# Optimization experiments

Measured on AMD Instinct MI355X. Metric: run time of the kernel, lower is better.

## Reference

```python
import jax, jax.numpy as jnp
import numpy as np
import math

B, S, H = 2, 2048, 3072
N_HEADS, N_KV_HEADS, HEAD_DIM = 32, 8, 96
ROPE_THETA = 10000.0
OP_SIZE = N_HEADS * HEAD_DIM + 2 * N_KV_HEADS * HEAD_DIM  # 4608


def setup_inputs() -> dict:
    key = jax.random.key(0)
    k1, k2, k3 = jax.random.split(key, 3)
    hidden_states = jax.random.normal(k1, (B, S, H), dtype=jnp.float32)
    # additive causal mask: 0 on/below diagonal, -inf-ish above
    neg = jnp.finfo(jnp.float32).min
    causal = jnp.where(jnp.tril(jnp.ones((S, S), dtype=bool)), 0.0, neg)
    attention_mask = jnp.broadcast_to(causal[None, None], (B, 1, S, S)).astype(jnp.float32)
    # torch nn.Linear convention: weight [out_features, in_features]
    w_qkv = jax.random.normal(k2, (OP_SIZE, H), dtype=jnp.float32) * 0.02
    w_o = jax.random.normal(k3, (H, H), dtype=jnp.float32) * 0.02
    position_ids = jnp.broadcast_to(jnp.arange(S, dtype=jnp.int32)[None], (B, S))
    return {"hidden_states": hidden_states, "attention_mask": attention_mask,
            "w_qkv": w_qkv, "w_o": w_o, "position_ids": position_ids}


def _rotate_half(x):
    half = x.shape[-1] // 2
    return jnp.concatenate([-x[..., half:], x[..., :half]], axis=-1)


def _rope_cos_sin(position_ids, head_dim, theta):
    # Phi3RotaryEmbedding (no scaling)
    inv_freq = 1.0 / (theta ** (jnp.arange(0, head_dim, 2, dtype=jnp.float32) / head_dim))
    freqs = position_ids.astype(jnp.float32)[:, :, None] * inv_freq[None, None, :]  # [b,s,d/2]
    emb = jnp.concatenate([freqs, freqs], axis=-1)  # [b,s,d]
    return jnp.cos(emb), jnp.sin(emb)


def reference(hidden_states, attention_mask, w_qkv, w_o, position_ids):
    b, s, _ = hidden_states.shape
    qkv = jnp.einsum('bsh,oh->bso', hidden_states, w_qkv)  # quantized qkv_proj (fp emulation)
    q_pos = N_HEADS * HEAD_DIM
    kv_pos = q_pos + N_KV_HEADS * HEAD_DIM
    q = qkv[..., :q_pos].reshape(b, s, N_HEADS, HEAD_DIM).transpose(0, 2, 1, 3)
    k = qkv[..., q_pos:kv_pos].reshape(b, s, N_KV_HEADS, HEAD_DIM).transpose(0, 2, 1, 3)
    v = qkv[..., kv_pos:].reshape(b, s, N_KV_HEADS, HEAD_DIM).transpose(0, 2, 1, 3)

    cos, sin = _rope_cos_sin(position_ids, HEAD_DIM, ROPE_THETA)
    cos, sin = cos[:, None], sin[:, None]  # [b,1,s,d]
    q = q * cos + _rotate_half(q) * sin
    k = k * cos + _rotate_half(k) * sin

    # repeat_kv: GQA expand kv heads to query heads
    groups = N_HEADS // N_KV_HEADS
    k = jnp.repeat(k, groups, axis=1)  # [b,h,s,d]
    v = jnp.repeat(v, groups, axis=1)

    # quantized QK^T matmul (fp emulation)
    scores = jnp.einsum('bhqd,bhkd->bhqk', q, k) / math.sqrt(HEAD_DIM)
    scores = scores + attention_mask  # additive causal mask
    attn = jax.nn.softmax(scores.astype(jnp.float32), axis=-1).astype(v.dtype)
    # dropout p=0 (eval); quantized attn @ V matmul (fp emulation)
    out = jnp.einsum('bhqk,bhkd->bhqd', attn, v)
    out = out.transpose(0, 2, 1, 3).reshape(b, s, N_HEADS * HEAD_DIM)
    out = jnp.einsum('bso,ho->bsh', out, w_o)  # quantized o_proj
    return out
```

## Files before the change

kernel.cpp:

```cpp
#include <hip/hip_runtime.h>
#include <hip/hip_bf16.h>
#include <math.h>

#define S_LEN 2048
#define HDIM  3072
#define NH    32
#define NKV   8
#define HD    96
#define OPSZ  4608
#define QPOS  3072
#define KPOS  3840

typedef short  short8 __attribute__((ext_vector_type(8)));
typedef short  short4v __attribute__((ext_vector_type(4)));
typedef float  f32x4  __attribute__((ext_vector_type(4)));
typedef unsigned short us4 __attribute__((ext_vector_type(4)));

typedef __attribute__((address_space(1))) const unsigned int* gas1_t;
typedef __attribute__((address_space(3))) unsigned int* las3_t;

__device__ __forceinline__ void gl_lds16(const void* g, void* l) {
  __builtin_amdgcn_global_load_lds((gas1_t)g, (las3_t)l, 16, 0, 0);
}

__device__ __forceinline__ unsigned short f2b(float f) {
  union { float f; unsigned u; } x; x.f = f;
  unsigned r = x.u + 0x7fffu + ((x.u >> 16) & 1u);
  return (unsigned short)(r >> 16);
}
__device__ __forceinline__ float b2f(unsigned short b) {
  union { unsigned u; float f; } x; x.u = ((unsigned)b) << 16;
  return x.f;
}

__device__ __forceinline__ short4v pack_bf16_4(float p0, float p1, float p2, float p3) {
  unsigned u0 = __builtin_bit_cast(unsigned, p0) + 0x8000u;
  unsigned u1 = __builtin_bit_cast(unsigned, p1) + 0x8000u;
  unsigned u2 = __builtin_bit_cast(unsigned, p2) + 0x8000u;
  unsigned u3 = __builtin_bit_cast(unsigned, p3) + 0x8000u;
  unsigned lo = __builtin_amdgcn_perm(u1, u0, 0x07060302u);
  unsigned hi = __builtin_amdgcn_perm(u3, u2, 0x07060302u);
  uint2 q; q.x = lo; q.y = hi;
  return __builtin_bit_cast(short4v, q);
}

__global__ __launch_bounds__(256) void k_convert(const float* __restrict__ src,
                                                 unsigned short* __restrict__ dst, int n4) {
  int i = blockIdx.x * 256 + threadIdx.x;
  if (i >= n4) return;
  float4 v = ((const float4*)src)[i];
  us4 o;
  o[0] = f2b(v.x); o[1] = f2b(v.y); o[2] = f2b(v.z); o[3] = f2b(v.w);
  ((us4*)dst)[i] = o;
}

template<int OUTBF>
__global__ __launch_bounds__(256) void k_gemm_bt(const unsigned short* __restrict__ A,
                                                 const unsigned short* __restrict__ Bt,
                                                 void* __restrict__ Cout,
                                                 int M, int N, int K) {
  __shared__ unsigned short As[128 * 64];
  __shared__ unsigned short Bs[128 * 64];
  const int tid  = threadIdx.x;
  const int lane = tid & 63;
  const int wave = tid >> 6;
  const int wm = wave & 1, wn = wave >> 1;
  const int lr = lane & 15, lg = lane >> 4;
  const int swz = lr & 7;
  const int m0 = blockIdx.y * 128, n0 = blockIdx.x * 128;

  f32x4 acc[4][4];
#pragma unroll
  for (int i = 0; i < 4; i++)
#pragma unroll
    for (int j = 0; j < 4; j++)
#pragma unroll
      for (int r = 0; r < 4; r++) acc[i][j][r] = 0.0f;

  for (int k0 = 0; k0 < K; k0 += 64) {
#pragma unroll
    for (int p = 0; p < 4; p++) {
      int gi  = p * 256 + tid;
      int row = gi >> 3, sg = gi & 7;
      int g   = sg ^ (row & 7);
      gl_lds16(A  + (size_t)(m0 + row) * K + k0 + g * 8, &As[row * 64 + sg * 8]);
      gl_lds16(Bt + (size_t)(n0 + row) * K + k0 + g * 8, &Bs[row * 64 + sg * 8]);
    }
    __syncthreads();
#pragma unroll
    for (int ks = 0; ks < 2; ks++) {
      short8 a[4], b[4];
#pragma unroll
      for (int mt = 0; mt < 4; mt++)
        a[mt] = *(const short8*)&As[(wm * 64 + mt * 16 + lr) * 64 + ((ks * 4 + lg) ^ swz) * 8];
#pragma unroll
      for (int nt = 0; nt < 4; nt++)
        b[nt] = *(const short8*)&Bs[(wn * 64 + nt * 16 + lr) * 64 + ((ks * 4 + lg) ^ swz) * 8];
#pragma unroll
      for (int mt = 0; mt < 4; mt++)
#pragma unroll
        for (int nt = 0; nt < 4; nt++)
          acc[mt][nt] = __builtin_amdgcn_mfma_f32_16x16x32_bf16(a[mt], b[nt], acc[mt][nt], 0, 0, 0);
    }
    __syncthreads();
  }

#pragma unroll
  for (int mt = 0; mt < 4; mt++)
#pragma unroll
    for (int nt = 0; nt < 4; nt++)
#pragma unroll
      for (int r = 0; r < 4; r++) {
        int row = m0 + wm * 64 + mt * 16 + lg * 4 + r;
        int col = n0 + wn * 64 + nt * 16 + lr;
        if (OUTBF) ((unsigned short*)Cout)[(size_t)row * N + col] = f2b(acc[mt][nt][r]);
        else       ((float*)Cout)[(size_t)row * N + col] = acc[mt][nt][r];
      }
}

__global__ __launch_bounds__(256) void k_rope(const unsigned short* __restrict__ qkv,
                                              const int* __restrict__ pos_ids,
                                              unsigned short* __restrict__ Qb,
                                              unsigned short* __restrict__ Kb) {
  __shared__ float cs[96], sn[96];
  int blk = blockIdx.x;
  int b = blk >> 11, s = blk & 2047;
  int t = threadIdx.x;
  int pos = pos_ids[blk];
  if (t < 48) {
    double e = -((double)(2 * t) / 96.0) * log(10000.0);
    float invf = (float)exp(e);
    float a = (float)pos * invf;
    float c, si;
    sincosf(a, &si, &c);
    cs[t] = c; cs[t + 48] = c;
    sn[t] = si; sn[t + 48] = si;
  }
  __syncthreads();
  const unsigned short* row = qkv + (size_t)blk * OPSZ;
  const float qscale = 0.1020620726159658f;
  for (int o = t; o < KPOS; o += 256) {
    int d = o % 96;
    float x  = b2f(row[o]);
    float xp = b2f(row[d < 48 ? o + 48 : o - 48]);
    float rot = (d < 48) ? -xp : xp;
    float val = x * cs[d] + rot * sn[d];
    if (o < QPOS) {
      int h = o / 96;
      Qb[((size_t)(b * NH + h) * S_LEN + s) * HD + d] = f2b(val * qscale);
    } else {
      int kh = (o - QPOS) / 96;
      Kb[((size_t)(b * NKV + kh) * S_LEN + s) * HD + d] = f2b(val);
    }
  }
}

__global__ __launch_bounds__(256) void k_vtrans(const unsigned short* __restrict__ qkv,
                                                unsigned short* __restrict__ Vt) {
  int blk = blockIdx.x;
  int st = blk & 31, kh = (blk >> 5) & 7, b = blk >> 8;
  int s0 = st * 64;
  __shared__ unsigned short tile[96][65];
  int t = threadIdx.x;
#pragma unroll
  for (int c = 0; c < 24; c++) {
    int idx = c * 256 + t;
    int ls = idx / 96, d = idx % 96;
    tile[d][ls] = qkv[(size_t)(b * S_LEN + s0 + ls) * OPSZ + KPOS + kh * 96 + d];
  }
  __syncthreads();
#pragma unroll
  for (int c = 0; c < 24; c++) {
    int idx = c * 256 + t;
    int d = idx >> 6, ls = idx & 63;
    Vt[((size_t)(b * NKV + kh) * HD + d) * S_LEN + s0 + ls] = tile[d][ls];
  }
}

__global__ __launch_bounds__(512, 4) void k_flash(const unsigned short* __restrict__ Qb,
                                                  const unsigned short* __restrict__ Kb,
                                                  const unsigned short* __restrict__ Vt,
                                                  unsigned short* __restrict__ attn) {
  __shared__ unsigned short smem[24832];
  __shared__ float Lsh[128 * 8];
  unsigned short* Ks  = smem;
  unsigned short* Vs  = smem + 6144;
  unsigned short* QPs = smem + 12288;
  float* Osh = (float*)smem;

  int blk = blockIdx.x;
  int j = blk & 7;
  int h = (blk >> 3) & 31;
  int b = blk >> 8;
  int kh = h >> 2;
  int tid = threadIdx.x, lane = tid & 63, wave = tid >> 6;
  int lr = lane & 15, lg = lane >> 4;
  int qg = wave >> 1, kg = wave & 1;
  const int swz = (lr >> 1) & 3;

  const unsigned short* ksrc = Kb + (size_t)(b * NKV + kh) * S_LEN * HD;
  const unsigned short* vsrc = Vt + (size_t)(b * NKV + kh) * HD * S_LEN;

  for (int half = 0; half < 2; half++) {
    int qtile = half ? (15 - j) : j;
    int q0 = qtile * 128;
    const unsigned short* qsrc = Qb + ((size_t)(b * NH + h) * S_LEN + q0) * HD;

    __syncthreads();
#pragma unroll
    for (int p = 0; p < 3; p++) {
      int gi = p * 512 + tid;
      int pl = gi >> 9, wp = gi & 511;
      int r = wp >> 2, s = wp & 3;
      int l = pl * 4 + (s ^ ((r >> 1) & 3));
      gl_lds16(qsrc + (size_t)r * HD + l * 8, &QPs[gi * 8]);
    }
#pragma unroll
    for (int p = 0; p < 3; p++) {
      int gi = p * 512 + tid;
      if (gi < 768) {
        int pl = gi >> 8, wp = gi & 255;
        int r = wp >> 2, s = wp & 3;
        int l = pl * 4 + (s ^ ((r >> 1) & 3));
        gl_lds16(ksrc + (size_t)r * HD + l * 8, &Ks[gi * 8]);
      } else {
        int gi2 = gi - 768;
        int pl = (gi2 >= 384) ? 1 : 0;
        int rem = gi2 - pl * 384;
        int d = rem >> 2, s = rem & 3;
        int l = s ^ ((d >> 1) & 3);
        gl_lds16(vsrc + (size_t)d * S_LEN + pl * 32 + l * 8, &Vs[gi2 * 8]);
      }
    }
    __syncthreads();

    short8 qf[2][3];
#pragma unroll
    for (int qt = 0; qt < 2; qt++)
#pragma unroll
      for (int ds = 0; ds < 3; ds++)
        qf[qt][ds] = *(const short8*)&QPs[ds * 4096 + (qg * 32 + qt * 16 + lr) * 32 + (lg ^ swz) * 8];

    f32x4 oacc[2][6];
#pragma unroll
    for (int qt = 0; qt < 2; qt++)
#pragma unroll
      for (int dt = 0; dt < 6; dt++)
#pragma unroll
        for (int r = 0; r < 4; r++) oacc[qt][dt][r] = 0.0f;
    float lsum[2] = {0.0f, 0.0f};

    int nk = qtile * 2 + 2;
    for (int it = 0; it < nk; it++) {
      int k0 = it * 64;
      f32x4 sc[2][2];
#pragma unroll
      for (int kt = 0; kt < 2; kt++)
#pragma unroll
        for (int qt = 0; qt < 2; qt++)
#pragma unroll
          for (int r = 0; r < 4; r++) sc[kt][qt][r] = 0.0f;
#pragma unroll
      for (int kt = 0; kt < 2; kt++)
#pragma unroll
        for (int ds = 0; ds < 3; ds++) {
          short8 kf = *(const short8*)&Ks[ds * 2048 + (kg * 32 + kt * 16 + lr) * 32 + (lg ^ swz) * 8];
#pragma unroll
          for (int qt = 0; qt < 2; qt++)
            sc[kt][qt] = __builtin_amdgcn_mfma_f32_16x16x32_bf16(kf, qf[qt][ds], sc[kt][qt], 0, 0, 0);
        }
      if (it >= nk - 2) {
#pragma unroll
        for (int kt = 0; kt < 2; kt++)
#pragma unroll
          for (int qt = 0; qt < 2; qt++) {
            int qrow = q0 + qg * 32 + qt * 16 + lr;
            int keyb = k0 + kg * 32 + kt * 16 + lg * 4;
#pragma unroll
            for (int r = 0; r < 4; r++)
              if (keyb + r > qrow) sc[kt][qt][r] = -3.0e38f;
          }
      }
      short4v pf[2][2];
#pragma unroll
      for (int kt = 0; kt < 2; kt++)
#pragma unroll
        for (int qt = 0; qt < 2; qt++) {
          float p0 = __expf(sc[kt][qt][0]);
          float p1 = __expf(sc[kt][qt][1]);
          float p2 = __expf(sc[kt][qt][2]);
          float p3 = __expf(sc[kt][qt][3]);
          lsum[qt] += (p0 + p1) + (p2 + p3);
          pf[kt][qt] = pack_bf16_4(p0, p1, p2, p3);
        }
#pragma unroll
      for (int kt = 0; kt < 2; kt++)
#pragma unroll
        for (int dt = 0; dt < 6; dt++) {
          short4v vf = *(const short4v*)&Vs[kg * 3072 + (dt * 16 + lr) * 32 +
                                           (((kt * 2 + (lg >> 1)) ^ swz) * 8) + (lg & 1) * 4];
#pragma unroll
          for (int qt = 0; qt < 2; qt++)
            oacc[qt][dt] = __builtin_amdgcn_mfma_f32_16x16x16bf16_1k(pf[kt][qt], vf, oacc[qt][dt], 0, 0, 0);
        }
      __syncthreads();
      if (it + 1 < nk) {
        int k0n = (it + 1) * 64;
#pragma unroll
        for (int p = 0; p < 3; p++) {
          int gi = p * 512 + tid;
          if (gi < 768) {
            int pl = gi >> 8, wp = gi & 255;
            int r = wp >> 2, s = wp & 3;
            int l = pl * 4 + (s ^ ((r >> 1) & 3));
            gl_lds16(ksrc + (size_t)(k0n + r) * HD + l * 8, &Ks[gi * 8]);
          } else {
            int gi2 = gi - 768;
            int pl = (gi2 >= 384) ? 1 : 0;
            int rem = gi2 - pl * 384;
            int d = rem >> 2, s = rem & 3;
            int l = s ^ ((d >> 1) & 3);
            gl_lds16(vsrc + (size_t)d * S_LEN + k0n + pl * 32 + l * 8, &Vs[gi2 * 8]);
          }
        }
        __syncthreads();
      }
    }
    if (kg == 0) {
#pragma unroll
      for (int qt = 0; qt < 2; qt++)
#pragma unroll
        for (int dt = 0; dt < 6; dt++)
#pragma unroll
          for (int r = 0; r < 4; r++)
            Osh[(qg * 32 + qt * 16 + lg * 4 + r) * 97 + dt * 16 + lr] = oacc[qt][dt][r];
    }
#pragma unroll
    for (int qt = 0; qt < 2; qt++)
      Lsh[(qg * 32 + qt * 16 + lr) * 8 + kg * 4 + lg] = lsum[qt];
    __syncthreads();
    if (kg == 1) {
      float linv[2][4];
#pragma unroll
      for (int qt = 0; qt < 2; qt++)
#pragma unroll
        for (int r = 0; r < 4; r++) {
          int row = qg * 32 + qt * 16 + lg * 4 + r;
          float4 a = *(const float4*)&Lsh[row * 8];
          float4 c = *(const float4*)&Lsh[row * 8 + 4];
          linv[qt][r] = 1.0f / ((a.x + a.y + a.z + a.w) + (c.x + c.y + c.z + c.w));
        }
#pragma unroll
      for (int qt = 0; qt < 2; qt++)
#pragma unroll
        for (int dt = 0; dt < 6; dt++)
#pragma unroll
          for (int r = 0; r < 4; r++) {
            int rowl = qg * 32 + qt * 16 + lg * 4 + r;
            float v = Osh[rowl * 97 + dt * 16 + lr] + oacc[qt][dt][r];
            int row = q0 + rowl;
            int col = h * 96 + dt * 16 + lr;
            attn[(size_t)(b * S_LEN + row) * HDIM + col] = f2b(v * linv[qt][r]);
          }
    }
  }
}

extern "C" void kernel_launch(void* const* d_in, const int* in_sizes, int n_in,
                              void* d_out, int out_size, void* d_ws, size_t ws_size,
                              hipStream_t stream) {
  const float* hidden = (const float*)d_in[0];
  const float* w_qkv  = (const float*)d_in[2];
  const float* w_o    = (const float*)d_in[3];
  const int*   posids = (const int*)d_in[4];

  const size_t M = 4096;
  unsigned short* hidden_bf = (unsigned short*)d_ws;
  unsigned short* wqkv_bf   = hidden_bf + M * HDIM;
  unsigned short* wo_bf     = wqkv_bf + (size_t)OPSZ * HDIM;
  unsigned short* qkv_bf    = wo_bf + (size_t)HDIM * HDIM;
  unsigned short* Qb   = hidden_bf;
  unsigned short* Kb   = wqkv_bf;
  unsigned short* Vt   = wqkv_bf + (size_t)NKV * 2 * S_LEN * HD;
  unsigned short* attn = qkv_bf;

  int n4h = (int)(M * HDIM / 4);
  int n4q = (int)((size_t)OPSZ * HDIM / 4);
  int n4o = (int)((size_t)HDIM * HDIM / 4);
  k_convert<<<(n4h + 255) / 256, 256, 0, stream>>>(hidden, hidden_bf, n4h);
  k_convert<<<(n4q + 255) / 256, 256, 0, stream>>>(w_qkv, wqkv_bf, n4q);
  k_convert<<<(n4o + 255) / 256, 256, 0, stream>>>(w_o, wo_bf, n4o);

  k_gemm_bt<1><<<dim3(OPSZ / 128, M / 128), 256, 0, stream>>>(hidden_bf, wqkv_bf, qkv_bf,
                                                              (int)M, OPSZ, HDIM);
  k_rope<<<(int)M, 256, 0, stream>>>(qkv_bf, posids, Qb, Kb);
  k_vtrans<<<2 * NKV * (S_LEN / 64), 256, 0, stream>>>(qkv_bf, Vt);
  k_flash<<<2 * NH * 8, 512, 0, stream>>>(Qb, Kb, Vt, attn);
  k_gemm_bt<0><<<dim3(HDIM / 128, M / 128), 256, 0, stream>>>(attn, wo_bf, d_out,
                                                              (int)M, HDIM, HDIM);
}
```

Baseline: 565.5 us.

## Replace GEMM with 4-stage pipelined 256x192 tile kernel with grid swizzle

Replaces the simple 128x128 synchronous-load GEMM with a 512-thread kernel that uses 256x192 tiles and a 4-slot LDS ring of 32-wide K chunks. Loads for chunk c+3 are issued while earlier chunks are computed, with explicit vmcnt waits, barriers and setprio around the MFMA blocks. Workgroup ids are remapped by an XCD-aware swizzle to improve L2 locality. The intent is to hide global-load latency and raise MFMA utilisation in both projections. The cost is a larger LDS footprint, more registers and fragile hand-tuned waitcnt logic that depends on the K size.

```diff
diff --git a/kernel.cpp b/kernel.cpp
--- a/kernel.cpp
+++ b/kernel.cpp
@@ -22,6 +22,8 @@
 __device__ __forceinline__ void gl_lds16(const void* g, void* l) {
   __builtin_amdgcn_global_load_lds((gas1_t)g, (las3_t)l, 16, 0, 0);
 }
+
+#define VMCNT(n) asm volatile("s_waitcnt vmcnt(" #n ")" ::: "memory")
 
 __device__ __forceinline__ unsigned short f2b(float f) {
   union { float f; unsigned u; } x; x.f = f;
@@ -54,67 +56,118 @@
   ((us4*)dst)[i] = o;
 }
 
+#define GSLOT 14336
 template<int OUTBF>
-__global__ __launch_bounds__(256) void k_gemm_bt(const unsigned short* __restrict__ A,
-                                                 const unsigned short* __restrict__ Bt,
-                                                 void* __restrict__ Cout,
-                                                 int M, int N, int K) {
-  __shared__ unsigned short As[128 * 64];
-  __shared__ unsigned short Bs[128 * 64];
-  const int tid  = threadIdx.x;
+__global__ __launch_bounds__(512, 2) void k_gemm_pipe(const unsigned short* __restrict__ A,
+                                                      const unsigned short* __restrict__ Bt,
+                                                      void* __restrict__ Cout,
+                                                      int M, int N, int K, int GX) {
+  __shared__ unsigned short lds[4 * GSLOT];
+
+  const int NC = K >> 5;
+  const int tid = threadIdx.x;
   const int lane = tid & 63;
   const int wave = tid >> 6;
-  const int wm = wave & 1, wn = wave >> 1;
+  const int wm = wave >> 2, wn = wave & 3;
   const int lr = lane & 15, lg = lane >> 4;
-  const int swz = lr & 7;
-  const int m0 = blockIdx.y * 128, n0 = blockIdx.x * 128;
-
-  f32x4 acc[4][4];
-#pragma unroll
-  for (int i = 0; i < 4; i++)
-#pragma unroll
-    for (int j = 0; j < 4; j++)
-#pragma unroll
-      for (int r = 0; r < 4; r++) acc[i][j][r] = 0.0f;
-
-  for (int k0 = 0; k0 < K; k0 += 64) {
-#pragma unroll
-    for (int p = 0; p < 4; p++) {
-      int gi  = p * 256 + tid;
-      int row = gi >> 3, sg = gi & 7;
-      int g   = sg ^ (row & 7);
-      gl_lds16(A  + (size_t)(m0 + row) * K + k0 + g * 8, &As[row * 64 + sg * 8]);
-      gl_lds16(Bt + (size_t)(n0 + row) * K + k0 + g * 8, &Bs[row * 64 + sg * 8]);
-    }
-    __syncthreads();
-#pragma unroll
-    for (int ks = 0; ks < 2; ks++) {
-      short8 a[4], b[4];
-#pragma unroll
-      for (int mt = 0; mt < 4; mt++)
-        a[mt] = *(const short8*)&As[(wm * 64 + mt * 16 + lr) * 64 + ((ks * 4 + lg) ^ swz) * 8];
-#pragma unroll
-      for (int nt = 0; nt < 4; nt++)
-        b[nt] = *(const short8*)&Bs[(wn * 64 + nt * 16 + lr) * 64 + ((ks * 4 + lg) ^ swz) * 8];
-#pragma unroll
-      for (int mt = 0; mt < 4; mt++)
-#pragma unroll
-        for (int nt = 0; nt < 4; nt++)
-          acc[mt][nt] = __builtin_amdgcn_mfma_f32_16x16x32_bf16(a[mt], b[nt], acc[mt][nt], 0, 0, 0);
-    }
-    __syncthreads();
-  }
-
-#pragma unroll
-  for (int mt = 0; mt < 4; mt++)
-#pragma unroll
-    for (int nt = 0; nt < 4; nt++)
+  const int prh = lr >> 1, bit = lr & 1;
+
+  const int nwg = gridDim.x;
+  const int id  = blockIdx.x;
+  const int sw  = (id & 7) * (nwg >> 3) + (id >> 3);
+  const int bx  = sw % GX, by = sw / GX;
+  const int m0 = by * 256, n0 = bx * 192;
+
+  const int i0 = tid, i1 = 512 + tid;
+  const int p0 = i0 >> 3, gl0 = (i0 & 7) ^ (p0 & 7);
+  const int p1 = i1 >> 3, gl1 = (i1 & 7) ^ (p1 & 7);
+  const unsigned short* aG0 = A + (size_t)(m0 + 2 * p0 + (gl0 >> 2)) * K + (gl0 & 3) * 8;
+  const unsigned short* aG1 = A + (size_t)(m0 + 2 * p1 + (gl1 >> 2)) * K + (gl1 & 3) * 8;
+  const int aO0 = i0 * 8, aO1 = i1 * 8;
+  const int q0 = i0 >> 3, hl0 = (i0 & 7) ^ (q0 & 7);
+  const int q1 = i1 >> 3, hl1 = (i1 & 7) ^ (q1 & 7);
+  const unsigned short* bG0 = Bt + (size_t)(n0 + 2 * q0 + (hl0 >> 2)) * K + (hl0 & 3) * 8;
+  const unsigned short* bG1 = Bt + (size_t)(n0 + 2 * q1 + (hl1 >> 2)) * K + (hl1 & 3) * 8;
+  const int bO0 = 8192 + i0 * 8, bO1 = 8192 + i1 * 8;
+  const bool loB2 = (tid < 256);
+
+  auto stageA = [&](int c) {
+    unsigned short* sb = &lds[(c & 3) * GSLOT];
+    gl_lds16(aG0 + c * 32, sb + aO0);
+    gl_lds16(aG1 + c * 32, sb + aO1);
+  };
+  auto stageB = [&](int c) {
+    unsigned short* sb = &lds[(c & 3) * GSLOT];
+    gl_lds16(bG0 + c * 32, sb + bO0);
+    if (loB2) gl_lds16(bG1 + c * 32, sb + bO1);
+  };
+
+  const int gp  = ((bit << 2) + lg) ^ prh;
+  const int aRd = wm * 4096 + prh * 64 + gp * 8;
+  const int bRd = 8192 + wn * 1536 + prh * 64 + gp * 8;
+
+  f32x4 acc[8][3];
+#pragma unroll
+  for (int mf = 0; mf < 8; mf++)
+#pragma unroll
+    for (int nf = 0; nf < 3; nf++)
+#pragma unroll
+      for (int r = 0; r < 4; r++) acc[mf][nf][r] = 0.0f;
+
+  stageA(0); stageB(0);
+  stageA(1); stageB(1);
+  stageA(2); stageB(2);
+  if (wave < 4) { VMCNT(8); } else { VMCNT(6); }
+  __builtin_amdgcn_s_barrier();
+  __builtin_amdgcn_sched_barrier(0);
+
+  for (int c = 0; c < NC; ++c) {
+    const unsigned short* sb = &lds[(c & 3) * GSLOT];
+    short8 af[4], bf[3];
+#pragma unroll
+    for (int mf = 0; mf < 4; mf++) af[mf] = *(const short8*)&sb[aRd + mf * 512];
+#pragma unroll
+    for (int nf = 0; nf < 3; nf++) bf[nf] = *(const short8*)&sb[bRd + nf * 512];
+    if (c + 3 < NC) stageA(c + 3);
+    __builtin_amdgcn_s_barrier();
+    __builtin_amdgcn_s_setprio(1);
+#pragma unroll
+    for (int mf = 0; mf < 4; mf++)
+#pragma unroll
+      for (int nf = 0; nf < 3; nf++)
+        acc[mf][nf] = __builtin_amdgcn_mfma_f32_16x16x32_bf16(af[mf], bf[nf], acc[mf][nf], 0, 0, 0);
+    __builtin_amdgcn_s_setprio(0);
+    __builtin_amdgcn_s_barrier();
+#pragma unroll
+    for (int mf = 0; mf < 4; mf++) af[mf] = *(const short8*)&sb[aRd + (4 + mf) * 512];
+    if (c + 3 < NC) stageB(c + 3);
+    __builtin_amdgcn_s_barrier();
+    __builtin_amdgcn_s_setprio(1);
+#pragma unroll
+    for (int mf = 0; mf < 4; mf++)
+#pragma unroll
+      for (int nf = 0; nf < 3; nf++)
+        acc[4 + mf][nf] = __builtin_amdgcn_mfma_f32_16x16x32_bf16(af[mf], bf[nf], acc[4 + mf][nf], 0, 0, 0);
+    __builtin_amdgcn_s_setprio(0);
+    if (c < NC - 3)        { if (wave < 4) { VMCNT(8); } else { VMCNT(6); } }
+    else if (c == NC - 3)  { if (wave < 4) { VMCNT(4); } else { VMCNT(3); } }
+    else if (c == NC - 2)  { VMCNT(0); }
+    if (c + 1 < NC) {
+      __builtin_amdgcn_s_barrier();
+      __builtin_amdgcn_sched_barrier(0);
+    }
+  }
+
+#pragma unroll
+  for (int mf = 0; mf < 8; mf++)
+#pragma unroll
+    for (int nf = 0; nf < 3; nf++)
 #pragma unroll
       for (int r = 0; r < 4; r++) {
-        int row = m0 + wm * 64 + mt * 16 + lg * 4 + r;
-        int col = n0 + wn * 64 + nt * 16 + lr;
-        if (OUTBF) ((unsigned short*)Cout)[(size_t)row * N + col] = f2b(acc[mt][nt][r]);
-        else       ((float*)Cout)[(size_t)row * N + col] = acc[mt][nt][r];
+        int row = m0 + wm * 128 + mf * 16 + lg * 4 + r;
+        int col = n0 + wn * 48 + nf * 16 + lr;
+        if (OUTBF) ((unsigned short*)Cout)[(size_t)row * N + col] = f2b(acc[mf][nf][r]);
+        else       ((float*)Cout)[(size_t)row * N + col] = acc[mf][nf][r];
       }
 }
 
@@ -391,11 +444,11 @@
   k_convert<<<(n4q + 255) / 256, 256, 0, stream>>>(w_qkv, wqkv_bf, n4q);
   k_convert<<<(n4o + 255) / 256, 256, 0, stream>>>(w_o, wo_bf, n4o);
 
-  k_gemm_bt<1><<<dim3(OPSZ / 128, M / 128), 256, 0, stream>>>(hidden_bf, wqkv_bf, qkv_bf,
-                                                              (int)M, OPSZ, HDIM);
+  k_gemm_pipe<1><<<384, 512, 0, stream>>>(hidden_bf, wqkv_bf, qkv_bf,
+                                          (int)M, OPSZ, HDIM, OPSZ / 192);
   k_rope<<<(int)M, 256, 0, stream>>>(qkv_bf, posids, Qb, Kb);
   k_vtrans<<<2 * NKV * (S_LEN / 64), 256, 0, stream>>>(qkv_bf, Vt);
   k_flash<<<2 * NH * 8, 512, 0, stream>>>(Qb, Kb, Vt, attn);
-  k_gemm_bt<0><<<dim3(HDIM / 128, M / 128), 256, 0, stream>>>(attn, wo_bf, d_out,
-                                                              (int)M, HDIM, HDIM);
-}
+  k_gemm_pipe<0><<<256, 512, 0, stream>>>(attn, wo_bf, d_out,
+                                          (int)M, HDIM, HDIM, HDIM / 192);
+}
```

Measured after the change: 545.8 us. 3.5% less time.
